# Kernel optimization log

Measured on AMD Instinct MI355X. Metric: run time of the kernel, lower is better.

Reference implementation:

```python
import jax, jax.numpy as jnp
import numpy as np

DIM = 1024
HEADS = 16
DIM_HEAD = 64
INNER = HEADS * DIM_HEAD  # 1024
MAX_LEN = 4096
BASE = 10000.0
EPS = 1.1920928955078125e-07  # torch.finfo(float32).eps (RMSNorm eps=None default)


def _rope_tables():
    t = np.arange(MAX_LEN, dtype=np.float32)
    inv_freq = 1.0 / (BASE ** (np.arange(0, DIM_HEAD, 2, dtype=np.float32) / DIM_HEAD))
    freqs = np.einsum('i,j->ij', t, inv_freq)          # [max_len, d/2]
    emb = np.concatenate([freqs, freqs], axis=-1)       # [max_len, d]
    return jnp.asarray(np.sin(emb)), jnp.asarray(np.cos(emb))


def setup_inputs() -> dict:
    key = jax.random.key(0)
    ks = jax.random.split(key, 5)
    x = jax.random.normal(ks[0], (2, 2048, DIM), dtype=jnp.float32)
    norm_w = jnp.ones((DIM,), dtype=jnp.float32)
    # store projection weights as [in, out] (transposed torch Linear weight)
    w_qkv = jax.random.normal(ks[1], (DIM, 3 * INNER), dtype=jnp.float32) * (DIM ** -0.5)
    w_o = jax.random.normal(ks[2], (INNER, DIM), dtype=jnp.float32) * (INNER ** -0.5)
    b_o = jax.random.normal(ks[3], (DIM,), dtype=jnp.float32) * 0.01
    sin, cos = _rope_tables()
    return {"x": x, "norm_w": norm_w, "w_qkv": w_qkv, "w_o": w_o, "b_o": b_o,
            "sin": sin, "cos": cos}


def _rotate_half(t):
    t1, t2 = jnp.split(t, 2, axis=-1)
    return jnp.concatenate([-t2, t1], axis=-1)


def _apply_rope(t, sin, cos):
    # t: [b, h, n, d]; sin/cos: [n, d]
    return t * cos + _rotate_half(t) * sin


def reference(x, norm_w, w_qkv, w_o, b_o, sin, cos):
    b, n, _ = x.shape
    # RMSNorm
    xn = x * jax.lax.rsqrt(jnp.mean(x * x, axis=-1, keepdims=True) + EPS) * norm_w
    # QKV projection
    qkv = xn @ w_qkv                                   # [b, n, 3*inner]
    q, k, v = jnp.split(qkv, 3, axis=-1)
    def to_heads(t):
        return t.reshape(b, n, HEADS, DIM_HEAD).transpose(0, 2, 1, 3)  # [b,h,n,d]
    q, k, v = to_heads(q), to_heads(k), to_heads(v)
    s, c = sin[:n], cos[:n]
    q = _apply_rope(q, s, c)
    k = _apply_rope(k, s, c)
    # causal SDPA
    scale = DIM_HEAD ** -0.5
    scores = jnp.einsum('bhqd,bhkd->bhqk', q, k) * scale
    causal = jnp.tril(jnp.ones((n, n), dtype=bool))
    scores = jnp.where(causal, scores, jnp.finfo(scores.dtype).min)
    attn = jax.nn.softmax(scores, axis=-1)
    out = jnp.einsum('bhqk,bhkd->bhqd', attn, v)
    out = out.transpose(0, 2, 1, 3).reshape(b, n, INNER)
    return out @ w_o + b_o
```

## Files before the change

kernel.cpp:

```cpp
#include <hip/hip_runtime.h>
#include <hip/hip_bf16.h>
#include <stdint.h>
#include <stddef.h>

#define NTOK   2048
#define NHEAD  16
#define DHEAD  64
#define DMODEL 1024
#define NROWS  4096
#define NQKV   3072
#define RMS_EPS 1.1920928955078125e-07f
#define QSCALE 0.1803368801111204f

typedef short bf16x8 __attribute__((ext_vector_type(8)));
typedef float f32x4  __attribute__((ext_vector_type(4)));
typedef unsigned short u16x4 __attribute__((ext_vector_type(4)));
typedef unsigned short u16x8 __attribute__((ext_vector_type(8)));

__device__ __forceinline__ unsigned short f2b(float f) {
  unsigned u = __builtin_bit_cast(unsigned, f);
  return (unsigned short)((u + 0x7fffu + ((u >> 16) & 1u)) >> 16);
}

__device__ __forceinline__ unsigned pk2bf(float a, float b) {
  __hip_bfloat162 h = __float22bfloat162_rn(make_float2(a, b));
  unsigned u;
  __builtin_memcpy(&u, &h, 4);
  return u;
}

__device__ __forceinline__ float fexp2(float x) {
#if __has_builtin(__builtin_amdgcn_exp2f)
  return __builtin_amdgcn_exp2f(x);
#else
  float r;
  asm("v_exp_f32 %0, %1" : "=v"(r) : "v"(x));
  return r;
#endif
}

__device__ __forceinline__ void gl16(const void* g, void* l) {
  __builtin_amdgcn_global_load_lds((__attribute__((address_space(1))) void*)g,
                                   (__attribute__((address_space(3))) void*)l,
                                   16, 0, 0);
}

__global__ __launch_bounds__(256) void k_rmsnorm(const float* __restrict__ x,
                                                 const float* __restrict__ w,
                                                 unsigned short* __restrict__ xn) {
  int row = blockIdx.x;
  int t = threadIdx.x;
  float4 v = ((const float4*)(x + (size_t)row * DMODEL))[t];
  float ss = v.x * v.x + v.y * v.y + v.z * v.z + v.w * v.w;
#pragma unroll
  for (int m = 1; m < 64; m <<= 1) ss += __shfl_xor(ss, m, 64);
  __shared__ float red[4];
  if ((t & 63) == 0) red[t >> 6] = ss;
  __syncthreads();
  float tot = (red[0] + red[1]) + (red[2] + red[3]);
  float rs = rsqrtf(tot * (1.0f / DMODEL) + RMS_EPS);
  float4 wv = ((const float4*)w)[t];
  u16x4 o;
  o.x = f2b(v.x * rs * wv.x);
  o.y = f2b(v.y * rs * wv.y);
  o.z = f2b(v.z * rs * wv.z);
  o.w = f2b(v.w * rs * wv.w);
  *(u16x4*)(xn + (size_t)row * DMODEL + t * 4) = o;
}

__global__ __launch_bounds__(256) void k_transpose_bf16(const float* __restrict__ W,
                                                        unsigned short* __restrict__ Wt,
                                                        int K, int Nw) {
  __shared__ float tile[64][65];
  int bk = blockIdx.x * 64;
  int bn = blockIdx.y * 64;
  int t = threadIdx.x;
  int tr = t >> 4;
  int tc = (t & 15) * 4;
#pragma unroll
  for (int rr = 0; rr < 64; rr += 16) {
    float4 v = *(const float4*)&W[(size_t)(bk + tr + rr) * Nw + bn + tc];
    tile[tr + rr][tc + 0] = v.x;
    tile[tr + rr][tc + 1] = v.y;
    tile[tr + rr][tc + 2] = v.z;
    tile[tr + rr][tc + 3] = v.w;
  }
  __syncthreads();
#pragma unroll
  for (int rr = 0; rr < 64; rr += 16) {
    int n = bn + tr + rr;
    u16x4 o;
    o.x = f2b(tile[tc + 0][tr + rr]);
    o.y = f2b(tile[tc + 1][tr + rr]);
    o.z = f2b(tile[tc + 2][tr + rr]);
    o.w = f2b(tile[tc + 3][tr + rr]);
    *(u16x4*)&Wt[(size_t)n * K + bk + tc] = o;
  }
}

#define QSTAGE(b, k0) do {                                   \
    gl16(Ag + (k0), &As[b][t * 8]);                          \
    gl16(Ag + (k0) + 64 * DMODEL, &As[b][(t + 256) * 8]);    \
    gl16(Bg + (k0), &Bs[b][t * 8]);                          \
    gl16(Bg + (k0) + 64 * DMODEL, &Bs[b][(t + 256) * 8]);    \
  } while (0)

__global__ __launch_bounds__(256) void k_qkv_gemm(
    const unsigned short* __restrict__ A, const unsigned short* __restrict__ Bt,
    const float* __restrict__ sin_t, const float* __restrict__ cos_t,
    unsigned short* __restrict__ Qh, unsigned short* __restrict__ Kh,
    unsigned short* __restrict__ VhT) {
  __shared__ unsigned short As[3][128 * 32];
  __shared__ unsigned short Bs[3][128 * 32];
  int bm = blockIdx.x, bn = blockIdx.y;
  int t = threadIdx.x;
  int l = t & 63, w = t >> 6;
  int wr = w >> 1, wc = w & 1;
  int lr = l & 15, lg = l >> 4;
  f32x4 acc[4][4] = {};

  int srow = t >> 2;
  int scho = ((t & 3) ^ ((t >> 3) & 3)) * 8;
  const unsigned short* Ag = A + (size_t)(bm * 128 + srow) * DMODEL + scho;
  const unsigned short* Bg = Bt + (size_t)(bn * 128 + srow) * DMODEL + scho;
  int swz = (lr >> 1) & 3;

  QSTAGE(0, 0);
  QSTAGE(1, 32);

  for (int i = 0; i < 32; i++) {
    int cb = i % 3;
    if (i < 31) { asm volatile("s_waitcnt vmcnt(4)" ::: "memory"); }
    else        { asm volatile("s_waitcnt vmcnt(0)" ::: "memory"); }
    __builtin_amdgcn_s_barrier();
    __builtin_amdgcn_sched_barrier(0);
    if (i < 30) QSTAGE((i + 2) % 3, (i + 2) * 32);
    bf16x8 af[4], bfr[4];
#pragma unroll
    for (int ii = 0; ii < 4; ii++)
      af[ii] = *(const bf16x8*)&As[cb][(wr * 64 + ii * 16 + lr) * 32 + (lg ^ swz) * 8];
#pragma unroll
    for (int jj = 0; jj < 4; jj++)
      bfr[jj] = *(const bf16x8*)&Bs[cb][(wc * 64 + jj * 16 + lr) * 32 + (lg ^ swz) * 8];
#pragma unroll
    for (int ii = 0; ii < 4; ii++)
#pragma unroll
      for (int jj = 0; jj < 4; jj++)
        acc[ii][jj] = __builtin_amdgcn_mfma_f32_16x16x32_bf16(af[ii], bfr[jj], acc[ii][jj], 0, 0, 0);
  }

  int nc0 = bn * 128 + wc * 64;
  int which = nc0 >> 10;
  int h = (nc0 & 1023) >> 6;
#pragma unroll
  for (int i = 0; i < 4; i++) {
#pragma unroll
    for (int r = 0; r < 4; r++) {
      int m = bm * 128 + wr * 64 + i * 16 + lg * 4 + r;
      int b = m >> 11;
      int n = m & (NTOK - 1);
      if (which == 2) {
#pragma unroll
        for (int j = 0; j < 4; j++) {
          int d = j * 16 + lr;
          VhT[((size_t)((b * NHEAD + h) * DHEAD) + d) * NTOK + n] = f2b(acc[i][j][r]);
        }
      } else {
        size_t obase = ((size_t)(b * NHEAD + h) * NTOK + n) * DHEAD;
        unsigned short* dst = which ? Kh : Qh;
        float qs = which ? 1.0f : QSCALE;
#pragma unroll
        for (int j = 0; j < 2; j++) {
          int d = j * 16 + lr;
          float t1 = acc[i][j][r];
          float t2 = acc[i][j + 2][r];
          float c1 = cos_t[n * DHEAD + d],      s1 = sin_t[n * DHEAD + d];
          float c2 = cos_t[n * DHEAD + d + 32], s2 = sin_t[n * DHEAD + d + 32];
          dst[obase + d]      = f2b((t1 * c1 - t2 * s1) * qs);
          dst[obase + d + 32] = f2b((t2 * c2 + t1 * s2) * qs);
        }
      }
    }
  }
}

#define SL(q, a, b) ((q) | ((a) << 6) | ((b) << 12))
__constant__ int SLOTS[48] = {
  SL(31,0,16), SL(31,16,32), SL(30,15,31), SL(15,0,16),
  SL(30,0,15), SL(29,0,15),  SL(29,15,30), SL(28,14,29), SL(14,0,15),
  SL(28,0,14), SL(27,0,14),  SL(27,14,28), SL(26,13,27), SL(13,0,14),
  SL(26,0,13), SL(25,0,13),  SL(25,13,26), SL(24,12,25), SL(12,0,13),
  SL(24,0,12), SL(23,0,12),  SL(23,12,24), SL(22,11,23), SL(11,0,12),
  SL(22,0,11), SL(21,0,11),  SL(21,11,22), SL(20,10,21), SL(10,0,11),
  SL(20,0,10), SL(19,0,10),  SL(19,10,20), SL(18,9,19),  SL(9,0,10),
  SL(18,0,9),  SL(17,0,9),   SL(17,9,18),  SL(16,8,17),  SL(8,0,9),
  SL(16,0,8),  SL(7,0,8),    SL(6,0,7),    SL(5,0,6),    SL(4,0,5),
  SL(3,0,4),   SL(2,0,3),    SL(1,0,2),    SL(0,0,1)
};

__global__ __launch_bounds__(256, 4) void k_attn(
    const unsigned short* __restrict__ Qh, const unsigned short* __restrict__ Kh,
    const unsigned short* __restrict__ VhT, unsigned short* __restrict__ AO,
    unsigned short* __restrict__ Opart, float* __restrict__ Mpart,
    float* __restrict__ Lpart) {
  int bh = blockIdx.x;
  int sv = SLOTS[blockIdx.y];
  int qt = sv & 63, kt0 = (sv >> 6) & 63, kt1 = sv >> 12;
  bool partial = (kt0 != 0) || (kt1 != qt + 1);
  int half = (kt0 != 0) ? 1 : 0;
  int t = threadIdx.x;
  int l = t & 63, w = t >> 6;
  int lr = l & 15, lg = l >> 4;

  __shared__ unsigned short Ks[2][64 * 64];
  __shared__ unsigned short Vs[2][64 * 64];
  __shared__ unsigned short Ps[4][16 * 64];

  const unsigned short* Qb = Qh  + (size_t)bh * NTOK * DHEAD;
  const unsigned short* Kb = Kh  + (size_t)bh * NTOK * DHEAD;
  const unsigned short* Vb = VhT + (size_t)bh * DHEAD * NTOK;

  int qrow = qt * 64 + w * 16 + lr;
  bf16x8 aq0 = *(const bf16x8*)&Qb[(size_t)qrow * DHEAD + lg * 8];
  bf16x8 aq1 = *(const bf16x8*)&Qb[(size_t)qrow * DHEAD + 32 + lg * 8];

  f32x4 accO[4] = {};
  float mrow = -1e38f;
  float lsum = 0.f;

  int srow = t >> 3;
  int spc  = t & 7;
  int sc0  = (spc ^ (srow & 7)) * 8;
  int sc1  = (spc ^ ((srow + 32) & 7)) * 8;

  int koff[4][2], voff[2][4], poff[2], pwoff[4];
#pragma unroll
  for (int nf = 0; nf < 4; nf++) {
    int krow = nf * 16 + lr;
    koff[nf][0] = krow * 128 + ((lg * 16) ^ ((krow & 7) << 4));
    koff[nf][1] = krow * 128 + ((lg * 16 + 64) ^ ((krow & 7) << 4));
    pwoff[nf] = lr * 128 + ((nf * 32 + lg * 8) ^ ((lr & 7) << 4));
  }
#pragma unroll
  for (int ks = 0; ks < 2; ks++) {
    poff[ks] = lr * 128 + ((lg * 16 + ks * 64) ^ ((lr & 7) << 4));
#pragma unroll
    for (int df = 0; df < 4; df++) {
      int col = df * 16 + lr;
      voff[ks][df] = col * 128 + ((lg * 16 + ks * 64) ^ ((col & 7) << 4));
    }
  }

  {
    int kv0 = kt0 * 64;
    gl16(Kb + (size_t)(kv0 + srow) * DHEAD + sc0, &Ks[0][t * 8]);
    gl16(Kb + (size_t)(kv0 + srow + 32) * DHEAD + sc1, &Ks[0][(t + 256) * 8]);
    gl16(Vb + (size_t)srow * NTOK + kv0 + sc0, &Vs[0][t * 8]);
    gl16(Vb + (size_t)(srow + 32) * NTOK + kv0 + sc1, &Vs[0][(t + 256) * 8]);
  }
  __syncthreads();

  for (int kt = kt0; kt < kt1; ++kt) {
    int cur = (kt - kt0) & 1, nxt = cur ^ 1;
    int kv0 = kt * 64;

    if (kt + 1 < kt1) {
      int kvn = kv0 + 64;
      gl16(Kb + (size_t)(kvn + srow) * DHEAD + sc0, &Ks[nxt][t * 8]);
      gl16(Kb + (size_t)(kvn + srow + 32) * DHEAD + sc1, &Ks[nxt][(t + 256) * 8]);
      gl16(Vb + (size_t)srow * NTOK + kvn + sc0, &Vs[nxt][t * 8]);
      gl16(Vb + (size_t)(srow + 32) * NTOK + kvn + sc1, &Vs[nxt][(t + 256) * 8]);
    }

    const char* kb = (const char*)Ks[cur];
    f32x4 s[4];
#pragma unroll
    for (int nf = 0; nf < 4; nf++) {
      bf16x8 bk0 = *(const bf16x8*)(kb + koff[nf][0]);
      bf16x8 bk1 = *(const bf16x8*)(kb + koff[nf][1]);
      f32x4 z = {};
      z = __builtin_amdgcn_mfma_f32_16x16x32_bf16(bk0, aq0, z, 0, 0, 0);
      s[nf] = __builtin_amdgcn_mfma_f32_16x16x32_bf16(bk1, aq1, z, 0, 0, 0);
    }

    if (kt == qt) {
      int qr = qt * 64 + w * 16 + lr;
#pragma unroll
      for (int nf = 0; nf < 4; nf++)
#pragma unroll
        for (int r = 0; r < 4; r++)
          if (kv0 + nf * 16 + lg * 4 + r > qr) s[nf][r] = -1e30f;
    }

    float t1m = fmaxf(fmaxf(s[0][0], s[0][1]), s[0][2]);
    float t2m = fmaxf(fmaxf(s[0][3], s[1][0]), s[1][1]);
    float t3m = fmaxf(fmaxf(s[1][2], s[1][3]), s[2][0]);
    float t4m = fmaxf(fmaxf(s[2][1], s[2][2]), s[2][3]);
    float t5m = fmaxf(fmaxf(s[3][0], s[3][1]), s[3][2]);
    float pm = fmaxf(fmaxf(fmaxf(t1m, t2m), t3m), fmaxf(fmaxf(t4m, t5m), s[3][3]));
    pm = fmaxf(pm, __shfl_xor(pm, 16, 64));
    pm = fmaxf(pm, __shfl_xor(pm, 32, 64));
    if (__any(pm > mrow + 8.0f)) {
      float mnew = fmaxf(mrow, pm);
      float corr = fexp2(mrow - mnew);
      mrow = mnew;
      lsum *= corr;
      float c0 = __shfl(corr, lg * 4 + 0, 64);
      float c1 = __shfl(corr, lg * 4 + 1, 64);
      float c2 = __shfl(corr, lg * 4 + 2, 64);
      float c3 = __shfl(corr, lg * 4 + 3, 64);
#pragma unroll
      for (int df = 0; df < 4; df++) {
        accO[df][0] *= c0; accO[df][1] *= c1;
        accO[df][2] *= c2; accO[df][3] *= c3;
      }
    }
    {
      float m = mrow;
      float sum = 0.f;
      char* pw = (char*)Ps[w];
#pragma unroll
      for (int nf = 0; nf < 4; nf++) {
        float p0 = fexp2(s[nf][0] - m);
        float p1 = fexp2(s[nf][1] - m);
        float p2 = fexp2(s[nf][2] - m);
        float p3 = fexp2(s[nf][3] - m);
        sum += (p0 + p1) + (p2 + p3);
        unsigned w0 = pk2bf(p0, p1);
        unsigned w1 = pk2bf(p2, p3);
        *(uint64_t*)(pw + pwoff[nf]) = (uint64_t)w0 | ((uint64_t)w1 << 32);
      }
      sum += __shfl_xor(sum, 16, 64);
      sum += __shfl_xor(sum, 32, 64);
      lsum += sum;
    }

    const char* pb = (const char*)Ps[w];
    const char* vb = (const char*)Vs[cur];
#pragma unroll
    for (int ks = 0; ks < 2; ks++) {
      bf16x8 ap = *(const bf16x8*)(pb + poff[ks]);
#pragma unroll
      for (int df = 0; df < 4; df++) {
        bf16x8 bv = *(const bf16x8*)(vb + voff[ks][df]);
        accO[df] = __builtin_amdgcn_mfma_f32_16x16x32_bf16(ap, bv, accO[df], 0, 0, 0);
      }
    }
    __syncthreads();
  }

  if (partial) {
    int pbase = (((bh << 4) + (qt - 16)) << 1) + half;
    if (lg == 0) {
      Mpart[pbase * 64 + w * 16 + lr] = mrow;
      Lpart[pbase * 64 + w * 16 + lr] = lsum;
    }
    unsigned short* Od = Opart + (size_t)pbase * 4096;
#pragma unroll
    for (int df = 0; df < 4; df++)
#pragma unroll
      for (int r = 0; r < 4; r++)
        Od[(w * 16 + lg * 4 + r) * 64 + df * 16 + lr] = f2b(accO[df][r]);
  } else {
    int b = bh >> 4, h = bh & 15;
    float li = 1.0f / lsum;
    float l0 = __shfl(li, lg * 4 + 0, 64);
    float l1 = __shfl(li, lg * 4 + 1, 64);
    float l2 = __shfl(li, lg * 4 + 2, 64);
    float l3 = __shfl(li, lg * 4 + 3, 64);
    int qbase = qt * 64 + w * 16;
#pragma unroll
    for (int df = 0; df < 4; df++) {
      int d = df * 16 + lr;
      size_t ob = ((size_t)(b * NTOK + qbase + lg * 4)) * DMODEL + h * DHEAD + d;
      AO[ob + 0 * DMODEL] = f2b(accO[df][0] * l0);
      AO[ob + 1 * DMODEL] = f2b(accO[df][1] * l1);
      AO[ob + 2 * DMODEL] = f2b(accO[df][2] * l2);
      AO[ob + 3 * DMODEL] = f2b(accO[df][3] * l3);
    }
  }
}

__global__ __launch_bounds__(256) void k_merge(const unsigned short* __restrict__ Opart,
                                               const float* __restrict__ Mpart,
                                               const float* __restrict__ Lpart,
                                               unsigned short* __restrict__ AO) {
  int bh = blockIdx.x, qq = blockIdx.y;
  int t = threadIdx.x;
  int row = t >> 2, d0 = (t & 3) << 4;
  int p0 = ((bh << 4) + qq) << 1;
  float m1 = Mpart[p0 * 64 + row],       l1 = Lpart[p0 * 64 + row];
  float m2 = Mpart[(p0 + 1) * 64 + row], l2 = Lpart[(p0 + 1) * 64 + row];
  float mm = fmaxf(m1, m2);
  float s1 = fexp2(m1 - mm), s2 = fexp2(m2 - mm);
  float li = 1.0f / (l1 * s1 + l2 * s2);
  float a1 = s1 * li, a2 = s2 * li;
  const unsigned short* O1 = Opart + (size_t)p0 * 4096 + row * 64 + d0;
  const unsigned short* O2 = O1 + 4096;
  int qt = 16 + qq;
  int b = bh >> 4, h = bh & 15;
  unsigned short* dst = AO + ((size_t)(b * NTOK + qt * 64 + row)) * DMODEL + h * DHEAD + d0;
#pragma unroll
  for (int c = 0; c < 2; c++) {
    u16x8 v1 = *(const u16x8*)(O1 + c * 8);
    u16x8 v2 = *(const u16x8*)(O2 + c * 8);
    u16x8 o;
#pragma unroll
    for (int e = 0; e < 8; e++) {
      float f1 = __builtin_bit_cast(float, (unsigned)v1[e] << 16);
      float g1 = __builtin_bit_cast(float, (unsigned)v2[e] << 16);
      o[e] = f2b(f1 * a1 + g1 * a2);
    }
    *(u16x8*)(dst + c * 8) = o;
  }
}

#define OSTAGE(b, k0) do {                                   \
    gl16(Ag + (k0), &As[b][t * 8]);                          \
    gl16(Ag + (k0) + 64 * DMODEL, &As[b][(t + 256) * 8]);    \
    gl16(Bg + (k0), &Bs[b][t * 8]);                          \
  } while (0)

__global__ __launch_bounds__(256) void k_out_gemm(
    const unsigned short* __restrict__ A, const unsigned short* __restrict__ Bt,
    const float* __restrict__ bias, float* __restrict__ out) {
  __shared__ unsigned short As[3][128 * 32];
  __shared__ unsigned short Bs[3][64 * 32];
  int bm = blockIdx.x, bn = blockIdx.y;
  int t = threadIdx.x;
  int l = t & 63, w = t >> 6;
  int wr = w >> 1, wc = w & 1;
  int lr = l & 15, lg = l >> 4;
  f32x4 acc[4][2] = {};

  int srow = t >> 2;
  int scho = ((t & 3) ^ ((t >> 3) & 3)) * 8;
  const unsigned short* Ag = A + (size_t)(bm * 128 + srow) * DMODEL + scho;
  const unsigned short* Bg = Bt + (size_t)(bn * 64 + srow) * DMODEL + scho;
  int swz = (lr >> 1) & 3;

  OSTAGE(0, 0);
  OSTAGE(1, 32);

  for (int i = 0; i < 32; i++) {
    int cb = i % 3;
    if (i < 31) { asm volatile("s_waitcnt vmcnt(3)" ::: "memory"); }
    else        { asm volatile("s_waitcnt vmcnt(0)" ::: "memory"); }
    __builtin_amdgcn_s_barrier();
    __builtin_amdgcn_sched_barrier(0);
    if (i < 30) OSTAGE((i + 2) % 3, (i + 2) * 32);
    bf16x8 af[4], bfr[2];
#pragma unroll
    for (int ii = 0; ii < 4; ii++)
      af[ii] = *(const bf16x8*)&As[cb][(wr * 64 + ii * 16 + lr) * 32 + (lg ^ swz) * 8];
#pragma unroll
    for (int jj = 0; jj < 2; jj++)
      bfr[jj] = *(const bf16x8*)&Bs[cb][(wc * 32 + jj * 16 + lr) * 32 + (lg ^ swz) * 8];
#pragma unroll
    for (int ii = 0; ii < 4; ii++)
#pragma unroll
      for (int jj = 0; jj < 2; jj++)
        acc[ii][jj] = __builtin_amdgcn_mfma_f32_16x16x32_bf16(af[ii], bfr[jj], acc[ii][jj], 0, 0, 0);
  }
  int nc0 = bn * 64 + wc * 32;
#pragma unroll
  for (int i = 0; i < 4; i++)
#pragma unroll
    for (int r = 0; r < 4; r++) {
      int m = bm * 128 + wr * 64 + i * 16 + lg * 4 + r;
      float* orow = out + (size_t)m * DMODEL;
#pragma unroll
      for (int j = 0; j < 2; j++) {
        int col = nc0 + j * 16 + lr;
        orow[col] = acc[i][j][r] + bias[col];
      }
    }
}

extern "C" void kernel_launch(void* const* d_in, const int* in_sizes, int n_in,
                              void* d_out, int out_size, void* d_ws, size_t ws_size,
                              hipStream_t stream) {
  const float* x      = (const float*)d_in[0];
  const float* norm_w = (const float*)d_in[1];
  const float* w_qkv  = (const float*)d_in[2];
  const float* w_o    = (const float*)d_in[3];
  const float* b_o    = (const float*)d_in[4];
  const float* sin_t  = (const float*)d_in[5];
  const float* cos_t  = (const float*)d_in[6];
  float* out = (float*)d_out;

  char* ws = (char*)d_ws;
  unsigned short* xn    = (unsigned short*)(ws + (0u << 20));
  unsigned short* wqkvT = (unsigned short*)(ws + (8u << 20));
  unsigned short* woT   = (unsigned short*)(ws + (14u << 20));
  unsigned short* Qh    = (unsigned short*)(ws + (16u << 20));
  unsigned short* Kh    = (unsigned short*)(ws + (24u << 20));
  unsigned short* VhT   = (unsigned short*)(ws + (32u << 20));
  unsigned short* AO    = (unsigned short*)(ws + (40u << 20));
  unsigned short* Opart = (unsigned short*)(ws + (0u << 20));
  float*          Mpart = (float*)(ws + (8u << 20));
  float*          Lpart = (float*)(ws + (8u << 20) + (1u << 18));

  hipLaunchKernelGGL(k_rmsnorm, dim3(NROWS), dim3(256), 0, stream, x, norm_w, xn);
  hipLaunchKernelGGL(k_transpose_bf16, dim3(16, 48), dim3(256), 0, stream, w_qkv, wqkvT, DMODEL, NQKV);
  hipLaunchKernelGGL(k_transpose_bf16, dim3(16, 16), dim3(256), 0, stream, w_o, woT, DMODEL, DMODEL);
  hipLaunchKernelGGL(k_qkv_gemm, dim3(32, 24), dim3(256), 0, stream, xn, wqkvT, sin_t, cos_t, Qh, Kh, VhT);
  hipLaunchKernelGGL(k_attn, dim3(32, 48), dim3(256), 0, stream, Qh, Kh, VhT, AO, Opart, Mpart, Lpart);
  hipLaunchKernelGGL(k_merge, dim3(32, 16), dim3(256), 0, stream, Opart, Mpart, Lpart, AO);
  hipLaunchKernelGGL(k_out_gemm, dim3(32, 16), dim3(256), 0, stream, AO, woT, b_o, out);
}
```

Measured before the change: 117.5 us.

## Retile QKV GEMM to 256x256 tiles with 8 waves and phased ping-pong scheduling

The QKV projection GEMM moves from 128x128 tiles with 4 waves and a 3-stage K=32 pipeline to 256x256 tiles with 8 waves, K=64 double buffering, and a four-phase loop. Each phase reads one fragment subset and issues the next stage's loads before running MFMAs under raised wave priority. s_setprio around MFMA blocks is also added in the attention and output GEMM kernels. This aims to raise data reuse per LDS byte and overlap loads with matrix math. The cost is a grid of only 192 blocks on 256 CUs, 128 KB of LDS per block, and more barriers per K step.

```diff
diff --git a/kernel.cpp b/kernel.cpp
--- a/kernel.cpp
+++ b/kernel.cpp
@@ -98,65 +98,123 @@
   }
 }
 
-#define QSTAGE(b, k0) do {                                   \
-    gl16(Ag + (k0), &As[b][t * 8]);                          \
-    gl16(Ag + (k0) + 64 * DMODEL, &As[b][(t + 256) * 8]);    \
-    gl16(Bg + (k0), &Bs[b][t * 8]);                          \
-    gl16(Bg + (k0) + 64 * DMODEL, &Bs[b][(t + 256) * 8]);    \
-  } while (0)
-
-__global__ __launch_bounds__(256) void k_qkv_gemm(
+__global__ __launch_bounds__(512, 2) void k_qkv_gemm(
     const unsigned short* __restrict__ A, const unsigned short* __restrict__ Bt,
     const float* __restrict__ sin_t, const float* __restrict__ cos_t,
     unsigned short* __restrict__ Qh, unsigned short* __restrict__ Kh,
     unsigned short* __restrict__ VhT) {
-  __shared__ unsigned short As[3][128 * 32];
-  __shared__ unsigned short Bs[3][128 * 32];
+  __shared__ unsigned short LA[2][256 * 64];
+  __shared__ unsigned short LB[2][256 * 64];
   int bm = blockIdx.x, bn = blockIdx.y;
   int t = threadIdx.x;
-  int l = t & 63, w = t >> 6;
-  int wr = w >> 1, wc = w & 1;
+  int wv = t >> 6, l = t & 63;
+  int wr = wv >> 2, wc = wv & 3;
   int lr = l & 15, lg = l >> 4;
-  f32x4 acc[4][4] = {};
-
-  int srow = t >> 2;
-  int scho = ((t & 3) ^ ((t >> 3) & 3)) * 8;
-  const unsigned short* Ag = A + (size_t)(bm * 128 + srow) * DMODEL + scho;
-  const unsigned short* Bg = Bt + (size_t)(bn * 128 + srow) * DMODEL + scho;
-  int swz = (lr >> 1) & 3;
-
-  QSTAGE(0, 0);
-  QSTAGE(1, 32);
-
-  for (int i = 0; i < 32; i++) {
-    int cb = i % 3;
-    if (i < 31) { asm volatile("s_waitcnt vmcnt(4)" ::: "memory"); }
-    else        { asm volatile("s_waitcnt vmcnt(0)" ::: "memory"); }
+  f32x4 acc[8][4] = {};
+
+  int strow = t >> 3;
+  int stch  = ((t & 7) ^ (strow & 7)) * 8;
+  const unsigned short* Ag = A  + (size_t)(bm * 256 + strow) * DMODEL + stch;
+  const unsigned short* Bg = Bt + (size_t)(bn * 256 + strow) * DMODEL + stch;
+  int sdst = strow * 64 + (t & 7) * 8;
+
+  int aswz = lr & 7;
+
+#define STAGE_A(kt) do { if ((kt) < 16) {                                   \
+    const unsigned short* g_ = Ag + (kt) * 64;                              \
+    unsigned short* d_ = LA[(kt) & 1];                                      \
+    gl16(g_,                        d_ + 0 * 4096 + sdst);                  \
+    gl16(g_ + (size_t) 64 * DMODEL, d_ + 1 * 4096 + sdst);                  \
+    gl16(g_ + (size_t)128 * DMODEL, d_ + 2 * 4096 + sdst);                  \
+    gl16(g_ + (size_t)192 * DMODEL, d_ + 3 * 4096 + sdst);                  \
+  } } while (0)
+#define STAGE_B(kt) do { if ((kt) < 16) {                                   \
+    const unsigned short* g_ = Bg + (kt) * 64;                              \
+    unsigned short* d_ = LB[(kt) & 1];                                      \
+    gl16(g_,                        d_ + 0 * 4096 + sdst);                  \
+    gl16(g_ + (size_t) 64 * DMODEL, d_ + 1 * 4096 + sdst);                  \
+    gl16(g_ + (size_t)128 * DMODEL, d_ + 2 * 4096 + sdst);                  \
+    gl16(g_ + (size_t)192 * DMODEL, d_ + 3 * 4096 + sdst);                  \
+  } } while (0)
+
+  STAGE_A(0);
+  STAGE_B(0);
+  asm volatile("s_waitcnt vmcnt(0)" ::: "memory");
+  __builtin_amdgcn_s_barrier();
+
+  bf16x8 af[4][2], bf0[2][2], bf1[2][2];
+
+#define RD_A(amh) do {                                                       \
+    _Pragma("unroll") for (int a2 = 0; a2 < 4; a2++) {                       \
+      int rowA = wr * 128 + ((amh) * 4 + a2) * 16 + lr;                      \
+      _Pragma("unroll") for (int kk = 0; kk < 2; kk++)                       \
+        af[a2][kk] = *(const bf16x8*)(pa + rowA * 128 +                      \
+                         (((kk * 4 + lg) ^ aswz) << 4));                     \
+    } } while (0)
+#define RD_B(dstf, bnh) do {                                                 \
+    _Pragma("unroll") for (int b2 = 0; b2 < 2; b2++) {                       \
+      int rowB = wc * 64 + ((bnh) * 2 + b2) * 16 + lr;                       \
+      _Pragma("unroll") for (int kk = 0; kk < 2; kk++)                       \
+        dstf[b2][kk] = *(const bf16x8*)(pb + rowB * 128 +                    \
+                         (((kk * 4 + lg) ^ aswz) << 4));                     \
+    } } while (0)
+#define MFMA16(amh, bfx, bnh) do {                                           \
+    _Pragma("unroll") for (int a2 = 0; a2 < 4; a2++)                         \
+      _Pragma("unroll") for (int b2 = 0; b2 < 2; b2++)                       \
+        _Pragma("unroll") for (int kk = 0; kk < 2; kk++)                     \
+          acc[(amh) * 4 + a2][(bnh) * 2 + b2] =                              \
+            __builtin_amdgcn_mfma_f32_16x16x32_bf16(af[a2][kk], bfx[b2][kk], \
+                acc[(amh) * 4 + a2][(bnh) * 2 + b2], 0, 0, 0);               \
+  } while (0)
+#define PHASE_SYNC() do {                                                    \
+    __builtin_amdgcn_s_barrier();                                            \
+    asm volatile("s_waitcnt lgkmcnt(0)" ::: "memory");                       \
+    __builtin_amdgcn_sched_barrier(0);                                       \
+    __builtin_amdgcn_s_setprio(1);                                           \
+  } while (0)
+
+  for (int kt = 0; kt < 16; ++kt) {
+    const char* pa = (const char*)LA[kt & 1];
+    const char* pb = (const char*)LB[kt & 1];
+    RD_A(0);
+    RD_B(bf0, 0);
+    STAGE_A(kt + 1);
+    PHASE_SYNC();
+    MFMA16(0, bf0, 0);
+    __builtin_amdgcn_s_setprio(0);
     __builtin_amdgcn_s_barrier();
-    __builtin_amdgcn_sched_barrier(0);
-    if (i < 30) QSTAGE((i + 2) % 3, (i + 2) * 32);
-    bf16x8 af[4], bfr[4];
-#pragma unroll
-    for (int ii = 0; ii < 4; ii++)
-      af[ii] = *(const bf16x8*)&As[cb][(wr * 64 + ii * 16 + lr) * 32 + (lg ^ swz) * 8];
-#pragma unroll
-    for (int jj = 0; jj < 4; jj++)
-      bfr[jj] = *(const bf16x8*)&Bs[cb][(wc * 64 + jj * 16 + lr) * 32 + (lg ^ swz) * 8];
-#pragma unroll
-    for (int ii = 0; ii < 4; ii++)
-#pragma unroll
-      for (int jj = 0; jj < 4; jj++)
-        acc[ii][jj] = __builtin_amdgcn_mfma_f32_16x16x32_bf16(af[ii], bfr[jj], acc[ii][jj], 0, 0, 0);
-  }
-
-  int nc0 = bn * 128 + wc * 64;
+    RD_B(bf1, 1);
+    STAGE_B(kt + 1);
+    PHASE_SYNC();
+    MFMA16(0, bf1, 1);
+    __builtin_amdgcn_s_setprio(0);
+    __builtin_amdgcn_s_barrier();
+    RD_A(1);
+    PHASE_SYNC();
+    MFMA16(1, bf1, 1);
+    __builtin_amdgcn_s_setprio(0);
+    __builtin_amdgcn_s_barrier();
+    PHASE_SYNC();
+    MFMA16(1, bf0, 0);
+    __builtin_amdgcn_s_setprio(0);
+    asm volatile("s_waitcnt vmcnt(0)" ::: "memory");
+    __builtin_amdgcn_s_barrier();
+  }
+#undef STAGE_A
+#undef STAGE_B
+#undef RD_A
+#undef RD_B
+#undef MFMA16
+#undef PHASE_SYNC
+
+  int nc0 = bn * 256 + wc * 64;
   int which = nc0 >> 10;
   int h = (nc0 & 1023) >> 6;
 #pragma unroll
-  for (int i = 0; i < 4; i++) {
+  for (int i = 0; i < 8; i++) {
 #pragma unroll
     for (int r = 0; r < 4; r++) {
-      int m = bm * 128 + wr * 64 + i * 16 + lg * 4 + r;
+      int m = bm * 256 + wr * 128 + i * 16 + lg * 4 + r;
       int b = m >> 11;
       int n = m & (NTOK - 1);
       if (which == 2) {
@@ -274,6 +332,7 @@
 
     const char* kb = (const char*)Ks[cur];
     f32x4 s[4];
+    __builtin_amdgcn_s_setprio(1);
 #pragma unroll
     for (int nf = 0; nf < 4; nf++) {
       bf16x8 bk0 = *(const bf16x8*)(kb + koff[nf][0]);
@@ -282,6 +341,7 @@
       z = __builtin_amdgcn_mfma_f32_16x16x32_bf16(bk0, aq0, z, 0, 0, 0);
       s[nf] = __builtin_amdgcn_mfma_f32_16x16x32_bf16(bk1, aq1, z, 0, 0, 0);
     }
+    __builtin_amdgcn_s_setprio(0);
 
     if (kt == qt) {
       int qr = qt * 64 + w * 16 + lr;
@@ -337,6 +397,7 @@
 
     const char* pb = (const char*)Ps[w];
     const char* vb = (const char*)Vs[cur];
+    __builtin_amdgcn_s_setprio(1);
 #pragma unroll
     for (int ks = 0; ks < 2; ks++) {
       bf16x8 ap = *(const bf16x8*)(pb + poff[ks]);
@@ -346,6 +407,7 @@
         accO[df] = __builtin_amdgcn_mfma_f32_16x16x32_bf16(ap, bv, accO[df], 0, 0, 0);
       }
     }
+    __builtin_amdgcn_s_setprio(0);
     __syncthreads();
   }
 
@@ -456,11 +518,13 @@
 #pragma unroll
     for (int jj = 0; jj < 2; jj++)
       bfr[jj] = *(const bf16x8*)&Bs[cb][(wc * 32 + jj * 16 + lr) * 32 + (lg ^ swz) * 8];
+    __builtin_amdgcn_s_setprio(1);
 #pragma unroll
     for (int ii = 0; ii < 4; ii++)
 #pragma unroll
       for (int jj = 0; jj < 2; jj++)
         acc[ii][jj] = __builtin_amdgcn_mfma_f32_16x16x32_bf16(af[ii], bfr[jj], acc[ii][jj], 0, 0, 0);
+    __builtin_amdgcn_s_setprio(0);
   }
   int nc0 = bn * 64 + wc * 32;
 #pragma unroll
@@ -504,7 +568,7 @@
   hipLaunchKernelGGL(k_rmsnorm, dim3(NROWS), dim3(256), 0, stream, x, norm_w, xn);
   hipLaunchKernelGGL(k_transpose_bf16, dim3(16, 48), dim3(256), 0, stream, w_qkv, wqkvT, DMODEL, NQKV);
   hipLaunchKernelGGL(k_transpose_bf16, dim3(16, 16), dim3(256), 0, stream, w_o, woT, DMODEL, DMODEL);
-  hipLaunchKernelGGL(k_qkv_gemm, dim3(32, 24), dim3(256), 0, stream, xn, wqkvT, sin_t, cos_t, Qh, Kh, VhT);
+  hipLaunchKernelGGL(k_qkv_gemm, dim3(16, 12), dim3(512), 0, stream, xn, wqkvT, sin_t, cos_t, Qh, Kh, VhT);
   hipLaunchKernelGGL(k_attn, dim3(32, 48), dim3(256), 0, stream, Qh, Kh, VhT, AO, Opart, Mpart, Lpart);
   hipLaunchKernelGGL(k_merge, dim3(32, 16), dim3(256), 0, stream, Opart, Mpart, Lpart, AO);
   hipLaunchKernelGGL(k_out_gemm, dim3(32, 16), dim3(256), 0, stream, AO, woT, b_o, out);
```

Measured after the change: 137.5 us. 1.17x slower.

## Enlarge attention query tile to 128 rows and rebalance causal split schedule

Applied to the files above, without the earlier changes.

The attention kernel now processes 128 query rows per block, two 16-row groups per wave, so each K/V tile loaded into shared memory feeds twice as many MFMAs. The work-slot table, the partial-output layout and the merge kernel are rebuilt for 128-row tiles, which halves the grid. s_setprio is also wrapped around the MFMA sections in the attention and output GEMM kernels. In exchange the kernel uses more registers and twice the P scratch in shared memory, and it drops the occupancy hint in launch bounds, which can lower occupancy. With half as many blocks, load balance across CUs may also get worse.

```diff
diff --git a/kernel.cpp b/kernel.cpp
--- a/kernel.cpp
+++ b/kernel.cpp
@@ -185,20 +185,19 @@
 }
 
 #define SL(q, a, b) ((q) | ((a) << 6) | ((b) << 12))
-__constant__ int SLOTS[48] = {
-  SL(31,0,16), SL(31,16,32), SL(30,15,31), SL(15,0,16),
-  SL(30,0,15), SL(29,0,15),  SL(29,15,30), SL(28,14,29), SL(14,0,15),
-  SL(28,0,14), SL(27,0,14),  SL(27,14,28), SL(26,13,27), SL(13,0,14),
-  SL(26,0,13), SL(25,0,13),  SL(25,13,26), SL(24,12,25), SL(12,0,13),
-  SL(24,0,12), SL(23,0,12),  SL(23,12,24), SL(22,11,23), SL(11,0,12),
-  SL(22,0,11), SL(21,0,11),  SL(21,11,22), SL(20,10,21), SL(10,0,11),
-  SL(20,0,10), SL(19,0,10),  SL(19,10,20), SL(18,9,19),  SL(9,0,10),
-  SL(18,0,9),  SL(17,0,9),   SL(17,9,18),  SL(16,8,17),  SL(8,0,9),
-  SL(16,0,8),  SL(7,0,8),    SL(6,0,7),    SL(5,0,6),    SL(4,0,5),
-  SL(3,0,4),   SL(2,0,3),    SL(1,0,2),    SL(0,0,1)
+__constant__ int SLOTS[24] = {
+  SL(15,0,16), SL(15,16,32), SL(7,0,16),
+  SL(14,0,15), SL(14,15,30),
+  SL(13,0,14), SL(13,14,28), SL(6,0,14),
+  SL(12,0,13), SL(12,13,26),
+  SL(11,0,12), SL(11,12,24), SL(5,0,12),
+  SL(10,0,11), SL(10,11,22),
+  SL(9,0,10),  SL(9,10,20),  SL(4,0,10),
+  SL(8,0,9),   SL(8,9,18),
+  SL(3,0,8),   SL(2,0,6),    SL(1,0,4),   SL(0,0,2)
 };
 
-__global__ __launch_bounds__(256, 4) void k_attn(
+__global__ __launch_bounds__(256) void k_attn(
     const unsigned short* __restrict__ Qh, const unsigned short* __restrict__ Kh,
     const unsigned short* __restrict__ VhT, unsigned short* __restrict__ AO,
     unsigned short* __restrict__ Opart, float* __restrict__ Mpart,
@@ -206,7 +205,7 @@
   int bh = blockIdx.x;
   int sv = SLOTS[blockIdx.y];
   int qt = sv & 63, kt0 = (sv >> 6) & 63, kt1 = sv >> 12;
-  bool partial = (kt0 != 0) || (kt1 != qt + 1);
+  bool partial = (kt0 != 0) || (kt1 != 2 * qt + 2);
   int half = (kt0 != 0) ? 1 : 0;
   int t = threadIdx.x;
   int l = t & 63, w = t >> 6;
@@ -214,36 +213,44 @@
 
   __shared__ unsigned short Ks[2][64 * 64];
   __shared__ unsigned short Vs[2][64 * 64];
-  __shared__ unsigned short Ps[4][16 * 64];
+  __shared__ unsigned short Ps[4][32 * 64];
 
   const unsigned short* Qb = Qh  + (size_t)bh * NTOK * DHEAD;
   const unsigned short* Kb = Kh  + (size_t)bh * NTOK * DHEAD;
   const unsigned short* Vb = VhT + (size_t)bh * DHEAD * NTOK;
 
-  int qrow = qt * 64 + w * 16 + lr;
-  bf16x8 aq0 = *(const bf16x8*)&Qb[(size_t)qrow * DHEAD + lg * 8];
-  bf16x8 aq1 = *(const bf16x8*)&Qb[(size_t)qrow * DHEAD + 32 + lg * 8];
-
-  f32x4 accO[4] = {};
-  float mrow = -1e38f;
-  float lsum = 0.f;
+  bf16x8 aq[2][2];
+#pragma unroll
+  for (int qg = 0; qg < 2; qg++) {
+    int qrow = qt * 128 + w * 32 + qg * 16 + lr;
+    aq[qg][0] = *(const bf16x8*)&Qb[(size_t)qrow * DHEAD + lg * 8];
+    aq[qg][1] = *(const bf16x8*)&Qb[(size_t)qrow * DHEAD + 32 + lg * 8];
+  }
+
+  f32x4 accO[2][4] = {};
+  float mrow[2] = {-1e38f, -1e38f};
+  float lsum[2] = {0.f, 0.f};
 
   int srow = t >> 3;
   int spc  = t & 7;
   int sc0  = (spc ^ (srow & 7)) * 8;
   int sc1  = (spc ^ ((srow + 32) & 7)) * 8;
 
-  int koff[4][2], voff[2][4], poff[2], pwoff[4];
+  int koff[4][2], voff[2][4], poff[2][2], pwoff[2][4];
 #pragma unroll
   for (int nf = 0; nf < 4; nf++) {
     int krow = nf * 16 + lr;
     koff[nf][0] = krow * 128 + ((lg * 16) ^ ((krow & 7) << 4));
     koff[nf][1] = krow * 128 + ((lg * 16 + 64) ^ ((krow & 7) << 4));
-    pwoff[nf] = lr * 128 + ((nf * 32 + lg * 8) ^ ((lr & 7) << 4));
+#pragma unroll
+    for (int qg = 0; qg < 2; qg++)
+      pwoff[qg][nf] = (qg * 16 + lr) * 128 + ((nf * 32 + lg * 8) ^ ((lr & 7) << 4));
   }
 #pragma unroll
   for (int ks = 0; ks < 2; ks++) {
-    poff[ks] = lr * 128 + ((lg * 16 + ks * 64) ^ ((lr & 7) << 4));
+#pragma unroll
+    for (int qg = 0; qg < 2; qg++)
+      poff[qg][ks] = (qg * 16 + lr) * 128 + ((lg * 16 + ks * 64) ^ ((lr & 7) << 4));
 #pragma unroll
     for (int df = 0; df < 4; df++) {
       int col = df * 16 + lr;
@@ -273,110 +280,131 @@
     }
 
     const char* kb = (const char*)Ks[cur];
-    f32x4 s[4];
+    f32x4 s[2][4];
+    __builtin_amdgcn_s_setprio(1);
 #pragma unroll
     for (int nf = 0; nf < 4; nf++) {
       bf16x8 bk0 = *(const bf16x8*)(kb + koff[nf][0]);
       bf16x8 bk1 = *(const bf16x8*)(kb + koff[nf][1]);
-      f32x4 z = {};
-      z = __builtin_amdgcn_mfma_f32_16x16x32_bf16(bk0, aq0, z, 0, 0, 0);
-      s[nf] = __builtin_amdgcn_mfma_f32_16x16x32_bf16(bk1, aq1, z, 0, 0, 0);
-    }
-
-    if (kt == qt) {
-      int qr = qt * 64 + w * 16 + lr;
-#pragma unroll
-      for (int nf = 0; nf < 4; nf++)
-#pragma unroll
-        for (int r = 0; r < 4; r++)
-          if (kv0 + nf * 16 + lg * 4 + r > qr) s[nf][r] = -1e30f;
-    }
-
-    float t1m = fmaxf(fmaxf(s[0][0], s[0][1]), s[0][2]);
-    float t2m = fmaxf(fmaxf(s[0][3], s[1][0]), s[1][1]);
-    float t3m = fmaxf(fmaxf(s[1][2], s[1][3]), s[2][0]);
-    float t4m = fmaxf(fmaxf(s[2][1], s[2][2]), s[2][3]);
-    float t5m = fmaxf(fmaxf(s[3][0], s[3][1]), s[3][2]);
-    float pm = fmaxf(fmaxf(fmaxf(t1m, t2m), t3m), fmaxf(fmaxf(t4m, t5m), s[3][3]));
-    pm = fmaxf(pm, __shfl_xor(pm, 16, 64));
-    pm = fmaxf(pm, __shfl_xor(pm, 32, 64));
-    if (__any(pm > mrow + 8.0f)) {
-      float mnew = fmaxf(mrow, pm);
-      float corr = fexp2(mrow - mnew);
-      mrow = mnew;
-      lsum *= corr;
-      float c0 = __shfl(corr, lg * 4 + 0, 64);
-      float c1 = __shfl(corr, lg * 4 + 1, 64);
-      float c2 = __shfl(corr, lg * 4 + 2, 64);
-      float c3 = __shfl(corr, lg * 4 + 3, 64);
-#pragma unroll
-      for (int df = 0; df < 4; df++) {
-        accO[df][0] *= c0; accO[df][1] *= c1;
-        accO[df][2] *= c2; accO[df][3] *= c3;
-      }
-    }
-    {
-      float m = mrow;
+#pragma unroll
+      for (int qg = 0; qg < 2; qg++) {
+        f32x4 z = {};
+        z = __builtin_amdgcn_mfma_f32_16x16x32_bf16(bk0, aq[qg][0], z, 0, 0, 0);
+        s[qg][nf] = __builtin_amdgcn_mfma_f32_16x16x32_bf16(bk1, aq[qg][1], z, 0, 0, 0);
+      }
+    }
+    __builtin_amdgcn_s_setprio(0);
+
+    if (kv0 + 63 > qt * 128 + w * 32) {
+#pragma unroll
+      for (int qg = 0; qg < 2; qg++) {
+        int qr = qt * 128 + w * 32 + qg * 16 + lr;
+#pragma unroll
+        for (int nf = 0; nf < 4; nf++)
+#pragma unroll
+          for (int r = 0; r < 4; r++)
+            if (kv0 + nf * 16 + lg * 4 + r > qr) s[qg][nf][r] = -1e30f;
+      }
+    }
+
+#pragma unroll
+    for (int qg = 0; qg < 2; qg++) {
+      float t1m = fmaxf(fmaxf(s[qg][0][0], s[qg][0][1]), s[qg][0][2]);
+      float t2m = fmaxf(fmaxf(s[qg][0][3], s[qg][1][0]), s[qg][1][1]);
+      float t3m = fmaxf(fmaxf(s[qg][1][2], s[qg][1][3]), s[qg][2][0]);
+      float t4m = fmaxf(fmaxf(s[qg][2][1], s[qg][2][2]), s[qg][2][3]);
+      float t5m = fmaxf(fmaxf(s[qg][3][0], s[qg][3][1]), s[qg][3][2]);
+      float pm = fmaxf(fmaxf(fmaxf(t1m, t2m), t3m), fmaxf(fmaxf(t4m, t5m), s[qg][3][3]));
+      pm = fmaxf(pm, __shfl_xor(pm, 16, 64));
+      pm = fmaxf(pm, __shfl_xor(pm, 32, 64));
+      if (__any(pm > mrow[qg] + 8.0f)) {
+        float mnew = fmaxf(mrow[qg], pm);
+        float corr = fexp2(mrow[qg] - mnew);
+        mrow[qg] = mnew;
+        lsum[qg] *= corr;
+        float c0 = __shfl(corr, lg * 4 + 0, 64);
+        float c1 = __shfl(corr, lg * 4 + 1, 64);
+        float c2 = __shfl(corr, lg * 4 + 2, 64);
+        float c3 = __shfl(corr, lg * 4 + 3, 64);
+#pragma unroll
+        for (int df = 0; df < 4; df++) {
+          accO[qg][df][0] *= c0; accO[qg][df][1] *= c1;
+          accO[qg][df][2] *= c2; accO[qg][df][3] *= c3;
+        }
+      }
+      float m = mrow[qg];
       float sum = 0.f;
       char* pw = (char*)Ps[w];
 #pragma unroll
       for (int nf = 0; nf < 4; nf++) {
-        float p0 = fexp2(s[nf][0] - m);
-        float p1 = fexp2(s[nf][1] - m);
-        float p2 = fexp2(s[nf][2] - m);
-        float p3 = fexp2(s[nf][3] - m);
+        float p0 = fexp2(s[qg][nf][0] - m);
+        float p1 = fexp2(s[qg][nf][1] - m);
+        float p2 = fexp2(s[qg][nf][2] - m);
+        float p3 = fexp2(s[qg][nf][3] - m);
         sum += (p0 + p1) + (p2 + p3);
         unsigned w0 = pk2bf(p0, p1);
         unsigned w1 = pk2bf(p2, p3);
-        *(uint64_t*)(pw + pwoff[nf]) = (uint64_t)w0 | ((uint64_t)w1 << 32);
+        *(uint64_t*)(pw + pwoff[qg][nf]) = (uint64_t)w0 | ((uint64_t)w1 << 32);
       }
       sum += __shfl_xor(sum, 16, 64);
       sum += __shfl_xor(sum, 32, 64);
-      lsum += sum;
+      lsum[qg] += sum;
     }
 
     const char* pb = (const char*)Ps[w];
     const char* vb = (const char*)Vs[cur];
+    __builtin_amdgcn_s_setprio(1);
 #pragma unroll
     for (int ks = 0; ks < 2; ks++) {
-      bf16x8 ap = *(const bf16x8*)(pb + poff[ks]);
+      bf16x8 ap0 = *(const bf16x8*)(pb + poff[0][ks]);
+      bf16x8 ap1 = *(const bf16x8*)(pb + poff[1][ks]);
 #pragma unroll
       for (int df = 0; df < 4; df++) {
         bf16x8 bv = *(const bf16x8*)(vb + voff[ks][df]);
-        accO[df] = __builtin_amdgcn_mfma_f32_16x16x32_bf16(ap, bv, accO[df], 0, 0, 0);
-      }
-    }
+        accO[0][df] = __builtin_amdgcn_mfma_f32_16x16x32_bf16(ap0, bv, accO[0][df], 0, 0, 0);
+        accO[1][df] = __builtin_amdgcn_mfma_f32_16x16x32_bf16(ap1, bv, accO[1][df], 0, 0, 0);
+      }
+    }
+    __builtin_amdgcn_s_setprio(0);
     __syncthreads();
   }
 
   if (partial) {
-    int pbase = (((bh << 4) + (qt - 16)) << 1) + half;
-    if (lg == 0) {
-      Mpart[pbase * 64 + w * 16 + lr] = mrow;
-      Lpart[pbase * 64 + w * 16 + lr] = lsum;
-    }
-    unsigned short* Od = Opart + (size_t)pbase * 4096;
-#pragma unroll
-    for (int df = 0; df < 4; df++)
-#pragma unroll
-      for (int r = 0; r < 4; r++)
-        Od[(w * 16 + lg * 4 + r) * 64 + df * 16 + lr] = f2b(accO[df][r]);
+    int pbase = ((bh << 3) + (qt - 8)) * 2 + half;
+#pragma unroll
+    for (int qg = 0; qg < 2; qg++) {
+      if (lg == 0) {
+        Mpart[pbase * 128 + w * 32 + qg * 16 + lr] = mrow[qg];
+        Lpart[pbase * 128 + w * 32 + qg * 16 + lr] = lsum[qg];
+      }
+    }
+    unsigned short* Od = Opart + (size_t)pbase * 8192;
+#pragma unroll
+    for (int qg = 0; qg < 2; qg++)
+#pragma unroll
+      for (int df = 0; df < 4; df++)
+#pragma unroll
+        for (int r = 0; r < 4; r++)
+          Od[(w * 32 + qg * 16 + lg * 4 + r) * 64 + df * 16 + lr] = f2b(accO[qg][df][r]);
   } else {
     int b = bh >> 4, h = bh & 15;
-    float li = 1.0f / lsum;
-    float l0 = __shfl(li, lg * 4 + 0, 64);
-    float l1 = __shfl(li, lg * 4 + 1, 64);
-    float l2 = __shfl(li, lg * 4 + 2, 64);
-    float l3 = __shfl(li, lg * 4 + 3, 64);
-    int qbase = qt * 64 + w * 16;
-#pragma unroll
-    for (int df = 0; df < 4; df++) {
-      int d = df * 16 + lr;
-      size_t ob = ((size_t)(b * NTOK + qbase + lg * 4)) * DMODEL + h * DHEAD + d;
-      AO[ob + 0 * DMODEL] = f2b(accO[df][0] * l0);
-      AO[ob + 1 * DMODEL] = f2b(accO[df][1] * l1);
-      AO[ob + 2 * DMODEL] = f2b(accO[df][2] * l2);
-      AO[ob + 3 * DMODEL] = f2b(accO[df][3] * l3);
+#pragma unroll
+    for (int qg = 0; qg < 2; qg++) {
+      float li = 1.0f / lsum[qg];
+      float l0 = __shfl(li, lg * 4 + 0, 64);
+      float l1 = __shfl(li, lg * 4 + 1, 64);
+      float l2 = __shfl(li, lg * 4 + 2, 64);
+      float l3 = __shfl(li, lg * 4 + 3, 64);
+      int qbase = qt * 128 + w * 32 + qg * 16;
+#pragma unroll
+      for (int df = 0; df < 4; df++) {
+        int d = df * 16 + lr;
+        size_t ob = ((size_t)(b * NTOK + qbase + lg * 4)) * DMODEL + h * DHEAD + d;
+        AO[ob + 0 * DMODEL] = f2b(accO[qg][df][0] * l0);
+        AO[ob + 1 * DMODEL] = f2b(accO[qg][df][1] * l1);
+        AO[ob + 2 * DMODEL] = f2b(accO[qg][df][2] * l2);
+        AO[ob + 3 * DMODEL] = f2b(accO[qg][df][3] * l3);
+      }
     }
   }
 }
@@ -387,21 +415,20 @@
                                                unsigned short* __restrict__ AO) {
   int bh = blockIdx.x, qq = blockIdx.y;
   int t = threadIdx.x;
-  int row = t >> 2, d0 = (t & 3) << 4;
-  int p0 = ((bh << 4) + qq) << 1;
-  float m1 = Mpart[p0 * 64 + row],       l1 = Lpart[p0 * 64 + row];
-  float m2 = Mpart[(p0 + 1) * 64 + row], l2 = Lpart[(p0 + 1) * 64 + row];
+  int row = t >> 1, d0 = (t & 1) << 5;
+  int p0 = ((bh << 3) + qq) << 1;
+  float m1 = Mpart[p0 * 128 + row],       l1 = Lpart[p0 * 128 + row];
+  float m2 = Mpart[(p0 + 1) * 128 + row], l2 = Lpart[(p0 + 1) * 128 + row];
   float mm = fmaxf(m1, m2);
   float s1 = fexp2(m1 - mm), s2 = fexp2(m2 - mm);
   float li = 1.0f / (l1 * s1 + l2 * s2);
   float a1 = s1 * li, a2 = s2 * li;
-  const unsigned short* O1 = Opart + (size_t)p0 * 4096 + row * 64 + d0;
-  const unsigned short* O2 = O1 + 4096;
-  int qt = 16 + qq;
+  const unsigned short* O1 = Opart + (size_t)p0 * 8192 + row * 64 + d0;
+  const unsigned short* O2 = O1 + 8192;
   int b = bh >> 4, h = bh & 15;
-  unsigned short* dst = AO + ((size_t)(b * NTOK + qt * 64 + row)) * DMODEL + h * DHEAD + d0;
-#pragma unroll
-  for (int c = 0; c < 2; c++) {
+  unsigned short* dst = AO + ((size_t)(b * NTOK + (qq + 8) * 128 + row)) * DMODEL + h * DHEAD + d0;
+#pragma unroll
+  for (int c = 0; c < 4; c++) {
     u16x8 v1 = *(const u16x8*)(O1 + c * 8);
     u16x8 v2 = *(const u16x8*)(O2 + c * 8);
     u16x8 o;
@@ -456,11 +483,13 @@
 #pragma unroll
     for (int jj = 0; jj < 2; jj++)
       bfr[jj] = *(const bf16x8*)&Bs[cb][(wc * 32 + jj * 16 + lr) * 32 + (lg ^ swz) * 8];
+    __builtin_amdgcn_s_setprio(1);
 #pragma unroll
     for (int ii = 0; ii < 4; ii++)
 #pragma unroll
       for (int jj = 0; jj < 2; jj++)
         acc[ii][jj] = __builtin_amdgcn_mfma_f32_16x16x32_bf16(af[ii], bfr[jj], acc[ii][jj], 0, 0, 0);
+    __builtin_amdgcn_s_setprio(0);
   }
   int nc0 = bn * 64 + wc * 32;
 #pragma unroll
@@ -505,7 +534,7 @@
   hipLaunchKernelGGL(k_transpose_bf16, dim3(16, 48), dim3(256), 0, stream, w_qkv, wqkvT, DMODEL, NQKV);
   hipLaunchKernelGGL(k_transpose_bf16, dim3(16, 16), dim3(256), 0, stream, w_o, woT, DMODEL, DMODEL);
   hipLaunchKernelGGL(k_qkv_gemm, dim3(32, 24), dim3(256), 0, stream, xn, wqkvT, sin_t, cos_t, Qh, Kh, VhT);
-  hipLaunchKernelGGL(k_attn, dim3(32, 48), dim3(256), 0, stream, Qh, Kh, VhT, AO, Opart, Mpart, Lpart);
-  hipLaunchKernelGGL(k_merge, dim3(32, 16), dim3(256), 0, stream, Opart, Mpart, Lpart, AO);
+  hipLaunchKernelGGL(k_attn, dim3(32, 24), dim3(256), 0, stream, Qh, Kh, VhT, AO, Opart, Mpart, Lpart);
+  hipLaunchKernelGGL(k_merge, dim3(32, 8), dim3(256), 0, stream, Opart, Mpart, Lpart, AO);
   hipLaunchKernelGGL(k_out_gemm, dim3(32, 16), dim3(256), 0, stream, AO, woT, b_o, out);
 }
```

Measured after the change: 127.6 us. +8.6%, slower.
